# Optimization experiments

Measured on AMD Instinct MI355X. Metric: run time of the kernel, lower is better.

The kernel has to match this reference:

```python
import jax, jax.numpy as jnp
import numpy as np

B, S, TAGSET = 64, 512, 62
T = TAGSET + 2  # + START (index T-2) and END (index T-1)


def setup_inputs() -> dict:
    key = jax.random.key(0)
    k1, k2, k3, k4 = jax.random.split(key, 4)
    feats = jax.random.normal(k1, (B, S, T), dtype=jnp.float32)
    # transitions param (torch init is zeros; small random for a non-degenerate baseline)
    transitions = 0.01 * jax.random.normal(k2, (T, T), dtype=jnp.float32)
    # variable-length contiguous-prefix mask (CRF assumes mask[:, 0] == 1)
    lengths = jax.random.randint(k3, (B,), S // 2, S + 1)
    mask = (jnp.arange(S)[None, :] < lengths[:, None]).astype(jnp.int32)
    tags = jax.random.randint(k4, (B, S), 0, TAGSET).astype(jnp.int32)
    return {"feats": feats, "transitions": transitions, "mask": mask, "tags": tags}


def _nll(feats, transitions, mask, tags):
    b, s, t = feats.shape
    maskb = mask.astype(bool)
    feats_t = jnp.transpose(feats, (1, 0, 2))  # [S, B, T]
    mask_t = jnp.transpose(maskb, (1, 0))       # [S, B]

    # ---- partition function (calculate_PZ) ----
    start = t - 2
    init_part = feats_t[0] + transitions[start][None, :]  # [B, T]

    def step(part, inp):
        f_t, m_t = inp  # f_t: [B, T] emissions, m_t: [B]
        # scores[b, i, j] = part[b, i] + transitions[i, j] + f_t[b, j]
        cur = jax.nn.logsumexp(
            part[:, :, None] + transitions[None, :, :] + f_t[:, None, :], axis=1
        )  # [B, T]
        part = jnp.where(m_t[:, None], cur, part)
        return part, None

    part, _ = jax.lax.scan(step, init_part, (feats_t[1:], mask_t[1:]))
    final = jax.nn.logsumexp(part[:, :, None] + transitions[None, :, :], axis=1)
    forward_score = final[:, t - 1].sum()  # transition into END

    # ---- gold score (score_sentence) ----
    tags = tags.astype(jnp.int32)
    prev = jnp.concatenate(
        [jnp.full((b, 1), start, dtype=jnp.int32), tags[:, :-1]], axis=1
    )  # [B, S] previous tag (START at t=0)
    emit = jnp.take_along_axis(feats, tags[..., None].astype(jnp.int32), axis=2)[..., 0]
    trans = transitions[prev, tags]  # [B, S]
    tg_energy = jnp.where(maskb, emit + trans, 0.0).sum()
    lengths = mask.astype(jnp.int32).sum(axis=1)  # [B]
    end_ids = jnp.take_along_axis(tags, (lengths - 1)[:, None], axis=1)[:, 0]
    end_energy = transitions[end_ids, t - 1].sum()
    gold_score = tg_energy + end_energy

    return forward_score - gold_score


def reference(feats, transitions, mask, tags):
    return _nll(feats, transitions, mask, tags)
```

## Files before the change

### kernel.cpp

```cpp
#include <hip/hip_runtime.h>


#define SS 512
#define TT 64
#define CC 8
#define KCH 64
#define START_TAG 62
#define END_TAG 63
#define LOG2E_F 1.44269504088896340736f
#define LN2_F 0.69314718055994530942f

#define WS_ECOL_OFF 4194304
#define MSTR 72

typedef float v4f __attribute__((ext_vector_type(4)));
typedef _Float16 h4 __attribute__((ext_vector_type(4)));
typedef __fp16 c2 __attribute__((ext_vector_type(2)));
union H4u { h4 v; struct { c2 lo, hi; } p; };

__device__ __forceinline__ void cstep(const h4 (&A)[4][4], h4 (&B)[4],
                                      float* __restrict__ emb, float& fq,
                                      const float* __restrict__ fcol, int tload,
                                      int q, int l, int& esum, int& esc) {
    v4f z = {0.f, 0.f, 0.f, 0.f};
    v4f D[4];
#pragma unroll
    for (int mt = 0; mt < 4; ++mt) {
        v4f a = __builtin_amdgcn_mfma_f32_16x16x16f16(A[mt][0], B[0], z, 0, 0, 0);
        a = __builtin_amdgcn_mfma_f32_16x16x16f16(A[mt][1], B[1], a, 0, 0, 0);
        v4f b = __builtin_amdgcn_mfma_f32_16x16x16f16(A[mt][2], B[2], z, 0, 0, 0);
        b = __builtin_amdgcn_mfma_f32_16x16x16f16(A[mt][3], B[3], b, 0, 0, 0);
        D[mt] = a + b;
    }
    v4f em[4];
#pragma unroll
    for (int mt = 0; mt < 4; ++mt) em[mt] = *(const v4f*)(emb + 16 * mt + 4 * q);
    emb[l] = __builtin_amdgcn_exp2f(fq * LOG2E_F);
    fq = fcol[(size_t)tload * TT];
    esum += esc;
    float scf = __uint_as_float((unsigned)(127 - esc) << 23);
    v4f qs[4];
#pragma unroll
    for (int mt = 0; mt < 4; ++mt) qs[mt] = D[mt] * (em[mt] * scf);
#pragma unroll
    for (int mt = 0; mt < 4; ++mt) {
        H4u u;
        u.p.lo = __builtin_amdgcn_cvt_pkrtz(qs[mt].x, qs[mt].y);
        u.p.hi = __builtin_amdgcn_cvt_pkrtz(qs[mt].z, qs[mt].w);
        B[mt] = u.v;
    }
    unsigned u0 = (unsigned)__builtin_amdgcn_readfirstlane((int)__float_as_uint(qs[0].x));
    esc = (int)((u0 >> 23) & 255u) - 127;
}

__global__ __launch_bounds__(256, 1)
void crf_chunks(const float* __restrict__ feats, const float* __restrict__ trans,
                const int* __restrict__ mask, unsigned short* __restrict__ Pg,
                int* __restrict__ Eg, float* __restrict__ out) {
    __shared__ float em[4][4][2][TT];
    __shared__ __align__(16) _Float16 mldB[TT * MSTR];
    __shared__ __align__(16) _Float16 mldD[TT * MSTR];
    __shared__ int ebuf[12];

    const int blk = blockIdx.x;
    const int chain = blk >> 3, c = blk & 7;
    const int tid = threadIdx.x;
    const int w = tid >> 6, l = tid & 63;
    const int n16 = l & 15, q = l >> 4;
    const int ncol = 16 * w + n16;

    if (blk == 0 && tid == 0) out[0] = 0.f;

    h4 A[4][4];
#pragma unroll
    for (int mt = 0; mt < 4; ++mt)
#pragma unroll
        for (int ks = 0; ks < 4; ++ks) {
            h4 a;
#pragma unroll
            for (int e = 0; e < 4; ++e)
                a[e] = (_Float16)__builtin_amdgcn_exp2f(
                    trans[(16 * ks + 4 * q + e) * TT + 16 * mt + n16] * LOG2E_F);
            A[mt][ks] = a;
        }

    const int* mp = mask + chain * SS;
    int msum = 0;
#pragma unroll
    for (int k = 0; k < 8; ++k) msum += mp[k * 64 + l];
#pragma unroll
    for (int s_ = 1; s_ < 64; s_ <<= 1) msum += __shfl_xor(msum, s_, 64);
    const int L = msum;

    const int t0a = 1 + KCH * c;
    const int t0b = t0a + 16, t0c = t0a + 32, t0d = t0a + 48;
    const int base = (L - 1) - KCH * c;
    int nA = base < 0 ? 0 : (base > 16 ? 16 : base);
    int nB = base - 16 < 0 ? 0 : (base - 16 > 16 ? 16 : base - 16);
    int nC = base - 32 < 0 ? 0 : (base - 32 > 16 ? 16 : base - 32);
    int nD = base - 48 < 0 ? 0 : (base - 48 > 16 ? 16 : base - 48);

    h4 Ba[4], Bb[4], Bc[4], Bd[4];
#pragma unroll
    for (int ks = 0; ks < 4; ++ks) {
        h4 b;
#pragma unroll
        for (int jj = 0; jj < 4; ++jj)
            b[jj] = (_Float16)((16 * ks + 4 * q + jj == ncol) ? 1.f : 0.f);
        Ba[ks] = b; Bb[ks] = b; Bc[ks] = b; Bd[ks] = b;
    }

    const float* fcol = feats + (size_t)chain * SS * TT + l;
#define CT(x) ((x) < SS ? (x) : SS - 1)
    em[0][w][0][l] = __builtin_amdgcn_exp2f(fcol[(size_t)CT(t0a) * TT] * LOG2E_F);
    em[0][w][1][l] = __builtin_amdgcn_exp2f(fcol[(size_t)CT(t0a + 1) * TT] * LOG2E_F);
    em[1][w][0][l] = __builtin_amdgcn_exp2f(fcol[(size_t)CT(t0b) * TT] * LOG2E_F);
    em[1][w][1][l] = __builtin_amdgcn_exp2f(fcol[(size_t)CT(t0b + 1) * TT] * LOG2E_F);
    em[2][w][0][l] = __builtin_amdgcn_exp2f(fcol[(size_t)CT(t0c) * TT] * LOG2E_F);
    em[2][w][1][l] = __builtin_amdgcn_exp2f(fcol[(size_t)CT(t0c + 1) * TT] * LOG2E_F);
    em[3][w][0][l] = __builtin_amdgcn_exp2f(fcol[(size_t)CT(t0d) * TT] * LOG2E_F);
    em[3][w][1][l] = __builtin_amdgcn_exp2f(fcol[(size_t)CT(t0d + 1) * TT] * LOG2E_F);
    float fqA0 = fcol[(size_t)CT(t0a + 2) * TT];
    float fqA1 = fcol[(size_t)CT(t0a + 3) * TT];
    float fqB0 = fcol[(size_t)CT(t0b + 2) * TT];
    float fqB1 = fcol[(size_t)CT(t0b + 3) * TT];
    float fqC0 = fcol[(size_t)CT(t0c + 2) * TT];
    float fqC1 = fcol[(size_t)CT(t0c + 3) * TT];
    float fqD0 = fcol[(size_t)CT(t0d + 2) * TT];
    float fqD1 = fcol[(size_t)CT(t0d + 3) * TT];

    int esA = 0, escA = 0, esB = 0, escB = 0;
    int esC = 0, escC = 0, esD = 0, escD = 0;

    if (nD == 16) {
        for (int r = 0; r < 8; ++r) {
            const int s0 = 2 * r;
            cstep(A, Ba, &em[0][w][0][0], fqA0, fcol, CT(t0a + s0 + 4), q, l, esA, escA);
            cstep(A, Bb, &em[1][w][0][0], fqB0, fcol, CT(t0b + s0 + 4), q, l, esB, escB);
            cstep(A, Bc, &em[2][w][0][0], fqC0, fcol, CT(t0c + s0 + 4), q, l, esC, escC);
            cstep(A, Bd, &em[3][w][0][0], fqD0, fcol, CT(t0d + s0 + 4), q, l, esD, escD);
            cstep(A, Ba, &em[0][w][1][0], fqA1, fcol, CT(t0a + s0 + 5), q, l, esA, escA);
            cstep(A, Bb, &em[1][w][1][0], fqB1, fcol, CT(t0b + s0 + 5), q, l, esB, escB);
            cstep(A, Bc, &em[2][w][1][0], fqC1, fcol, CT(t0c + s0 + 5), q, l, esC, escC);
            cstep(A, Bd, &em[3][w][1][0], fqD1, fcol, CT(t0d + s0 + 5), q, l, esD, escD);
        }
    } else {
        for (int r = 0; r < 8; ++r) {
            const int s0 = 2 * r, s1 = s0 + 1;
            if (s0 < nA) cstep(A, Ba, &em[0][w][0][0], fqA0, fcol, CT(t0a + s0 + 4), q, l, esA, escA);
            if (s0 < nB) cstep(A, Bb, &em[1][w][0][0], fqB0, fcol, CT(t0b + s0 + 4), q, l, esB, escB);
            if (s0 < nC) cstep(A, Bc, &em[2][w][0][0], fqC0, fcol, CT(t0c + s0 + 4), q, l, esC, escC);
            if (s0 < nD) cstep(A, Bd, &em[3][w][0][0], fqD0, fcol, CT(t0d + s0 + 4), q, l, esD, escD);
            if (s1 < nA) cstep(A, Ba, &em[0][w][1][0], fqA1, fcol, CT(t0a + s1 + 4), q, l, esA, escA);
            if (s1 < nB) cstep(A, Bb, &em[1][w][1][0], fqB1, fcol, CT(t0b + s1 + 4), q, l, esB, escB);
            if (s1 < nC) cstep(A, Bc, &em[2][w][1][0], fqC1, fcol, CT(t0c + s1 + 4), q, l, esC, escC);
            if (s1 < nD) cstep(A, Bd, &em[3][w][1][0], fqD1, fcol, CT(t0d + s1 + 4), q, l, esD, escD);
        }
    }
#undef CT

    if (l == 0) { ebuf[w] = esB; ebuf[4 + w] = esD; }
    __syncthreads();
    const int eBmax = max(max(ebuf[0], ebuf[1]), max(ebuf[2], ebuf[3]));
    const int eDmax = max(max(ebuf[4], ebuf[5]), max(ebuf[6], ebuf[7]));
    {
        _Float16 sB = (_Float16)ldexpf(1.f, esB - eBmax);
        _Float16 sD = (_Float16)ldexpf(1.f, esD - eDmax);
        h4 s4B = {sB, sB, sB, sB}, s4D = {sD, sD, sD, sD};
#pragma unroll
        for (int ks = 0; ks < 4; ++ks) {
            h4 vb = Bb[ks] * s4B;
            h4 vd = Bd[ks] * s4D;
#pragma unroll
            for (int jj = 0; jj < 4; ++jj) {
                mldB[(16 * ks + 4 * q + jj) * MSTR + ncol] = vb[jj];
                mldD[(16 * ks + 4 * q + jj) * MSTR + ncol] = vd[jj];
            }
        }
    }
    __syncthreads();
    h4 AHb[4][4], AHd[4][4];
#pragma unroll
    for (int mt = 0; mt < 4; ++mt)
#pragma unroll
        for (int ks = 0; ks < 4; ++ks) {
            AHb[mt][ks] = *(const h4*)(mldB + (16 * mt + n16) * MSTR + 16 * ks + 4 * q);
            AHd[mt][ks] = *(const h4*)(mldD + (16 * mt + n16) * MSTR + 16 * ks + 4 * q);
        }
    v4f z = {0.f, 0.f, 0.f, 0.f};
    v4f P1[4], P2[4];
#pragma unroll
    for (int mt = 0; mt < 4; ++mt) {
        v4f a = __builtin_amdgcn_mfma_f32_16x16x16f16(AHb[mt][0], Ba[0], z, 0, 0, 0);
        a = __builtin_amdgcn_mfma_f32_16x16x16f16(AHb[mt][1], Ba[1], a, 0, 0, 0);
        v4f b = __builtin_amdgcn_mfma_f32_16x16x16f16(AHb[mt][2], Ba[2], z, 0, 0, 0);
        b = __builtin_amdgcn_mfma_f32_16x16x16f16(AHb[mt][3], Ba[3], b, 0, 0, 0);
        P1[mt] = a + b;
        v4f a2 = __builtin_amdgcn_mfma_f32_16x16x16f16(AHd[mt][0], Bc[0], z, 0, 0, 0);
        a2 = __builtin_amdgcn_mfma_f32_16x16x16f16(AHd[mt][1], Bc[1], a2, 0, 0, 0);
        v4f b2 = __builtin_amdgcn_mfma_f32_16x16x16f16(AHd[mt][2], Bc[2], z, 0, 0, 0);
        b2 = __builtin_amdgcn_mfma_f32_16x16x16f16(AHd[mt][3], Bc[3], b2, 0, 0, 0);
        P2[mt] = a2 + b2;
    }
    float m1 = 0.f, m2 = 0.f;
#pragma unroll
    for (int mt = 0; mt < 4; ++mt) {
        m1 = fmaxf(m1, fmaxf(fmaxf(P1[mt].x, P1[mt].y), fmaxf(P1[mt].z, P1[mt].w)));
        m2 = fmaxf(m2, fmaxf(fmaxf(P2[mt].x, P2[mt].y), fmaxf(P2[mt].z, P2[mt].w)));
    }
#pragma unroll
    for (int m = 1; m < 64; m <<= 1) {
        m1 = fmaxf(m1, __shfl_xor(m1, m, 64));
        m2 = fmaxf(m2, __shfl_xor(m2, m, 64));
    }
    unsigned u1 = (unsigned)__builtin_amdgcn_readfirstlane((int)__float_as_uint(m1));
    unsigned u2 = (unsigned)__builtin_amdgcn_readfirstlane((int)__float_as_uint(m2));
    const int e1c = u1 ? (int)((u1 >> 23) & 255u) - 127 : 0;
    const int e2c = u2 ? (int)((u2 >> 23) & 255u) - 127 : 0;
    const int e1 = esA + eBmax + e1c;
    const int e2 = esC + eDmax + e2c;
    h4 P1h[4], P2h[4];
    {
        float s1f = __uint_as_float((unsigned)(127 - e1c) << 23);
        float s2f = __uint_as_float((unsigned)(127 - e2c) << 23);
#pragma unroll
        for (int mt = 0; mt < 4; ++mt) {
            v4f q1 = P1[mt] * s1f;
            v4f q2 = P2[mt] * s2f;
            H4u ua, ub;
            ua.p.lo = __builtin_amdgcn_cvt_pkrtz(q1.x, q1.y);
            ua.p.hi = __builtin_amdgcn_cvt_pkrtz(q1.z, q1.w);
            ub.p.lo = __builtin_amdgcn_cvt_pkrtz(q2.x, q2.y);
            ub.p.hi = __builtin_amdgcn_cvt_pkrtz(q2.z, q2.w);
            P1h[mt] = ua.v;
            P2h[mt] = ub.v;
        }
    }

    if (l == 0) ebuf[8 + w] = e2;
    __syncthreads();
    const int e2max = max(max(ebuf[8], ebuf[9]), max(ebuf[10], ebuf[11]));
    {
        _Float16 s2 = (_Float16)ldexpf(1.f, e2 - e2max);
        h4 s4 = {s2, s2, s2, s2};
#pragma unroll
        for (int mt = 0; mt < 4; ++mt) {
            h4 v = P2h[mt] * s4;
#pragma unroll
            for (int jj = 0; jj < 4; ++jj)
                mldB[(16 * mt + 4 * q + jj) * MSTR + ncol] = v[jj];
        }
    }
    __syncthreads();
    h4 AHp[4][4];
#pragma unroll
    for (int mt = 0; mt < 4; ++mt)
#pragma unroll
        for (int ks = 0; ks < 4; ++ks)
            AHp[mt][ks] = *(const h4*)(mldB + (16 * mt + n16) * MSTR + 16 * ks + 4 * q);
    h4 Rf[4];
#pragma unroll
    for (int mt = 0; mt < 4; ++mt) {
        v4f a = __builtin_amdgcn_mfma_f32_16x16x16f16(AHp[mt][0], P1h[0], z, 0, 0, 0);
        a = __builtin_amdgcn_mfma_f32_16x16x16f16(AHp[mt][1], P1h[1], a, 0, 0, 0);
        v4f b = __builtin_amdgcn_mfma_f32_16x16x16f16(AHp[mt][2], P1h[2], z, 0, 0, 0);
        b = __builtin_amdgcn_mfma_f32_16x16x16f16(AHp[mt][3], P1h[3], b, 0, 0, 0);
        v4f d = a + b;
        H4u u;
        u.p.lo = __builtin_amdgcn_cvt_pkrtz(d.x, d.y);
        u.p.hi = __builtin_amdgcn_cvt_pkrtz(d.z, d.w);
        Rf[mt] = u.v;
    }
#pragma unroll
    for (int mt = 0; mt < 4; ++mt)
#pragma unroll
        for (int jj = 0; jj < 4; ++jj)
            mldD[(16 * mt + 4 * q + jj) * MSTR + ncol] = Rf[mt][jj];
    __syncthreads();
    {
        const size_t base_ = ((size_t)chain * CC + c) * 4096;
        int r = tid >> 2, cb = tid & 3;
        const uint4* src = (const uint4*)(mldD + r * MSTR + cb * 16);
        uint4* dst = (uint4*)(Pg + base_ + r * TT + cb * 16);
        dst[0] = src[0];
        dst[1] = src[1];
    }
    if (q == 0) Eg[(chain * CC + c) * TT + ncol] = e1 + e2max;
}

__global__ __launch_bounds__(64, 1)
void crf_combine(const float* __restrict__ feats, const float* __restrict__ trans,
                 const int* __restrict__ mask, const int* __restrict__ tags,
                 const unsigned short* __restrict__ Pg, const int* __restrict__ Eg,
                 float* __restrict__ out) {
    __shared__ __align__(16) float yl[TT];
    const int chain = blockIdx.x;
    const int j = threadIdx.x;

    int msum = 0;
#pragma unroll
    for (int k = 0; k < 8; ++k) msum += mask[chain * SS + 64 * k + j];
#pragma unroll
    for (int m = 1; m < 64; m <<= 1) msum += __shfl_xor(msum, m, 64);
    const int L = msum;

    float g = 0.f;
#pragma unroll
    for (int k = 0; k < 8; ++k) {
        int t = 64 * k + j;
        if (t < L) {
            int cur = tags[chain * SS + t];
            int prev = t ? tags[chain * SS + t - 1] : START_TAG;
            g += feats[(size_t)chain * SS * TT + (size_t)t * TT + cur] + trans[prev * TT + cur];
        }
    }
#pragma unroll
    for (int m = 1; m < 64; m <<= 1) g += __shfl_xor(g, m, 64);

    float part0 = feats[(size_t)chain * SS * TT + j] + trans[START_TAG * TT + j];
    float M0 = part0;
#pragma unroll
    for (int m = 1; m < 64; m <<= 1) M0 = fmaxf(M0, __shfl_xor(M0, m, 64));
    float x = exp2f((part0 - M0) * LOG2E_F);
    int esumX = 0;

    for (int c = 0; c < CC; ++c) {
        int e = Eg[(chain * CC + c) * TT + j];
        int emax = e;
#pragma unroll
        for (int m = 1; m < 64; m <<= 1) emax = max(emax, __shfl_xor(emax, m, 64));
        yl[j] = ldexpf(x, e - emax);
        float yv[64];
        {
            const uint4* yq = (const uint4*)yl;
#pragma unroll
            for (int i = 0; i < 16; ++i) {
                union { uint4 u; float f[4]; } cv;
                cv.u = yq[i];
                yv[4 * i + 0] = cv.f[0]; yv[4 * i + 1] = cv.f[1];
                yv[4 * i + 2] = cv.f[2]; yv[4 * i + 3] = cv.f[3];
            }
        }
        const uint4* rp = (const uint4*)(Pg + ((size_t)chain * CC + c) * 4096 + (size_t)j * TT);
        float acc = 0.f;
#pragma unroll
        for (int i = 0; i < 8; ++i) {
            union { uint4 u; _Float16 h[8]; } pv;
            pv.u = rp[i];
#pragma unroll
            for (int k2 = 0; k2 < 8; ++k2)
                acc = __builtin_fmaf((float)pv.h[k2], yv[8 * i + k2], acc);
        }
        float am = acc;
#pragma unroll
        for (int m = 1; m < 64; m <<= 1) am = fmaxf(am, __shfl_xor(am, m, 64));
        int e0 = (int)((__float_as_uint(am) >> 23) & 255u) - 127;
        x = ldexpf(acc, -e0);
        esumX += e0 + emax;
    }

    float val = x * expf(trans[j * TT + END_TAG]);
#pragma unroll
    for (int m = 1; m < 64; m <<= 1) val += __shfl_xor(val, m, 64);
    float fwd = logf(val) + (float)esumX * LN2_F + M0;

    if (j == 0) {
        float gold = g + trans[tags[chain * SS + L - 1] * TT + END_TAG];
        atomicAdd(out, fwd - gold);
    }
}

extern "C" void kernel_launch(void* const* d_in, const int* in_sizes, int n_in,
                              void* d_out, int out_size, void* d_ws, size_t ws_size,
                              hipStream_t stream) {
    const float* feats = (const float*)d_in[0];
    const float* trans = (const float*)d_in[1];
    const int*   mask  = (const int*)d_in[2];
    const int*   tags  = (const int*)d_in[3];
    float* out = (float*)d_out;
    unsigned short* Pg = (unsigned short*)d_ws;
    int*       Eg = (int*)((char*)d_ws + WS_ECOL_OFF);

    crf_chunks<<<dim3(64 * CC), dim3(256), 0, stream>>>(feats, trans, mask, Pg, Eg, out);
    crf_combine<<<dim3(64), dim3(64), 0, stream>>>(feats, trans, mask, tags, Pg, Eg, out);
}
```

Before: 113.5 us.

## Combine chunk transfer matrices with an MFMA tree product across four waves

The combine kernel used to apply the eight per-chunk transfer matrices one after another as matrix-vector products in a single 64-thread wave. It now uses 256 threads and pairs chunk matrices with MFMA matrix-matrix products in a tree, staging through LDS and tracking per-column exponent rescaling, before a final reduction against the END weights. This shortens the serial dependency chain and puts the work on the matrix cores. In exchange it does more arithmetic, adds block barriers, and narrows intermediate products to fp16. The diff also leaves a redundant mask reduction and an odd no-op conditional when writing Eg.

Measured after the change: 119.5 us. 1.05x slower.

```diff
diff --git a/kernel.cpp b/kernel.cpp
--- a/kernel.cpp
+++ b/kernel.cpp
@@ -285,87 +285,280 @@
         dst[0] = src[0];
         dst[1] = src[1];
     }
-    if (q == 0) Eg[(chain * CC + c) * TT + ncol] = e1 + e2max;
-}
-
-__global__ __launch_bounds__(64, 1)
+    if (q == 0) Eg[(chain * CC + c) * TT + ncol] = e1 + eBmax == eBmax ? e1 + e2max : e1 + e2max;
+}
+
+__device__ __forceinline__ int wimax64(int v) {
+#pragma unroll
+    for (int m = 1; m < 64; m <<= 1) v = max(v, __shfl_xor(v, m, 64));
+    return v;
+}
+__device__ __forceinline__ float wfmax64(float v) {
+#pragma unroll
+    for (int m = 1; m < 64; m <<= 1) v = fmaxf(v, __shfl_xor(v, m, 64));
+    return v;
+}
+__device__ __forceinline__ float wfsum64(float v) {
+#pragma unroll
+    for (int m = 1; m < 64; m <<= 1) v += __shfl_xor(v, m, 64);
+    return v;
+}
+__device__ __forceinline__ int fexp(float m) {
+    unsigned u = (unsigned)__builtin_amdgcn_readfirstlane((int)__float_as_uint(m));
+    return u ? (int)((u >> 23) & 255u) - 127 : 0;
+}
+__device__ __forceinline__ void mm64(const h4 (&A)[4][4], const h4 (&B)[4], v4f (&D)[4]) {
+    v4f z = {0.f, 0.f, 0.f, 0.f};
+#pragma unroll
+    for (int mt = 0; mt < 4; ++mt) {
+        v4f a = __builtin_amdgcn_mfma_f32_16x16x16f16(A[mt][0], B[0], z, 0, 0, 0);
+        a = __builtin_amdgcn_mfma_f32_16x16x16f16(A[mt][1], B[1], a, 0, 0, 0);
+        v4f b = __builtin_amdgcn_mfma_f32_16x16x16f16(A[mt][2], B[2], z, 0, 0, 0);
+        b = __builtin_amdgcn_mfma_f32_16x16x16f16(A[mt][3], B[3], b, 0, 0, 0);
+        D[mt] = a + b;
+    }
+}
+__device__ __forceinline__ float dmax16(const v4f (&D)[4]) {
+    float m = 0.f;
+#pragma unroll
+    for (int mt = 0; mt < 4; ++mt)
+        m = fmaxf(m, fmaxf(fmaxf(D[mt].x, D[mt].y), fmaxf(D[mt].z, D[mt].w)));
+    return m;
+}
+__device__ __forceinline__ void prodG(const unsigned short* __restrict__ PgC, int cA, int cB,
+                                      const float* __restrict__ sAt,
+                                      int n16, int q, int ncol, v4f (&D)[4]) {
+    const _Float16* Ap = (const _Float16*)PgC + cA * 4096;
+    const _Float16* Bp = (const _Float16*)PgC + cB * 4096;
+    h4 Af[4][4];
+#pragma unroll
+    for (int mt = 0; mt < 4; ++mt)
+#pragma unroll
+        for (int ks = 0; ks < 4; ++ks) {
+            h4 raw = *(const h4*)(Ap + (16 * mt + n16) * TT + 16 * ks + 4 * q);
+            v4f s = *(const v4f*)(sAt + 16 * ks + 4 * q);
+            h4 a;
+#pragma unroll
+            for (int e = 0; e < 4; ++e) a[e] = (_Float16)((float)raw[e] * s[e]);
+            Af[mt][ks] = a;
+        }
+    h4 Bf[4];
+#pragma unroll
+    for (int ks = 0; ks < 4; ++ks) {
+        h4 b;
+#pragma unroll
+        for (int j = 0; j < 4; ++j) b[j] = Bp[(16 * ks + 4 * q + j) * TT + ncol];
+        Bf[ks] = b;
+    }
+    mm64(Af, Bf, D);
+}
+
+__global__ __launch_bounds__(256, 1)
 void crf_combine(const float* __restrict__ feats, const float* __restrict__ trans,
                  const int* __restrict__ mask, const int* __restrict__ tags,
                  const unsigned short* __restrict__ Pg, const int* __restrict__ Eg,
                  float* __restrict__ out) {
-    __shared__ __align__(16) float yl[TT];
+    __shared__ __align__(16) _Float16 stg[TT * MSTR];
+    __shared__ __align__(16) float sA[4][TT];
+    __shared__ __align__(16) float wend[TT];
+    __shared__ int eodd[4];
+    __shared__ int ib0[4], ib1[4], ib2[4], ib3[4];
+    __shared__ float redf[4], gred[4];
+
     const int chain = blockIdx.x;
-    const int j = threadIdx.x;
+    const int tid = threadIdx.x;
+    const int w = tid >> 6, l = tid & 63;
+    const int n16 = l & 15, q = l >> 4;
+    const int ncol = 16 * w + n16;
+    const unsigned short* PgC = Pg + (size_t)chain * CC * 4096;
+    const int* EgC = Eg + chain * CC * TT;
 
     int msum = 0;
 #pragma unroll
-    for (int k = 0; k < 8; ++k) msum += mask[chain * SS + 64 * k + j];
+    for (int k = 0; k < 8; ++k) msum += mask[chain * SS + 64 * k + l];
+    msum = wimax64(msum * 0 + msum);
+    msum = 0;
+#pragma unroll
+    for (int k = 0; k < 8; ++k) msum += mask[chain * SS + 64 * k + l];
 #pragma unroll
     for (int m = 1; m < 64; m <<= 1) msum += __shfl_xor(msum, m, 64);
     const int L = msum;
 
     float g = 0.f;
 #pragma unroll
-    for (int k = 0; k < 8; ++k) {
-        int t = 64 * k + j;
+    for (int rep = 0; rep < 2; ++rep) {
+        int t = tid + rep * 256;
         if (t < L) {
             int cur = tags[chain * SS + t];
             int prev = t ? tags[chain * SS + t - 1] : START_TAG;
             g += feats[(size_t)chain * SS * TT + (size_t)t * TT + cur] + trans[prev * TT + cur];
         }
     }
-#pragma unroll
-    for (int m = 1; m < 64; m <<= 1) g += __shfl_xor(g, m, 64);
-
-    float part0 = feats[(size_t)chain * SS * TT + j] + trans[START_TAG * TT + j];
-    float M0 = part0;
-#pragma unroll
-    for (int m = 1; m < 64; m <<= 1) M0 = fmaxf(M0, __shfl_xor(M0, m, 64));
-    float x = exp2f((part0 - M0) * LOG2E_F);
-    int esumX = 0;
-
-    for (int c = 0; c < CC; ++c) {
-        int e = Eg[(chain * CC + c) * TT + j];
-        int emax = e;
-#pragma unroll
-        for (int m = 1; m < 64; m <<= 1) emax = max(emax, __shfl_xor(emax, m, 64));
-        yl[j] = ldexpf(x, e - emax);
-        float yv[64];
-        {
-            const uint4* yq = (const uint4*)yl;
-#pragma unroll
-            for (int i = 0; i < 16; ++i) {
-                union { uint4 u; float f[4]; } cv;
-                cv.u = yq[i];
-                yv[4 * i + 0] = cv.f[0]; yv[4 * i + 1] = cv.f[1];
-                yv[4 * i + 2] = cv.f[2]; yv[4 * i + 3] = cv.f[3];
-            }
-        }
-        const uint4* rp = (const uint4*)(Pg + ((size_t)chain * CC + c) * 4096 + (size_t)j * TT);
-        float acc = 0.f;
-#pragma unroll
-        for (int i = 0; i < 8; ++i) {
-            union { uint4 u; _Float16 h[8]; } pv;
-            pv.u = rp[i];
-#pragma unroll
-            for (int k2 = 0; k2 < 8; ++k2)
-                acc = __builtin_fmaf((float)pv.h[k2], yv[8 * i + k2], acc);
-        }
-        float am = acc;
-#pragma unroll
-        for (int m = 1; m < 64; m <<= 1) am = fmaxf(am, __shfl_xor(am, m, 64));
-        int e0 = (int)((__float_as_uint(am) >> 23) & 255u) - 127;
-        x = ldexpf(acc, -e0);
-        esumX += e0 + emax;
-    }
-
-    float val = x * expf(trans[j * TT + END_TAG]);
-#pragma unroll
-    for (int m = 1; m < 64; m <<= 1) val += __shfl_xor(val, m, 64);
-    float fwd = logf(val) + (float)esumX * LN2_F + M0;
-
-    if (j == 0) {
-        float gold = g + trans[tags[chain * SS + L - 1] * TT + END_TAG];
+    g = wfsum64(g);
+    if (l == 0) gred[w] = g;
+
+    {
+        int e1 = EgC[(2 * w + 1) * TT + l];
+        int em = wimax64(e1);
+        if (l == 0) eodd[w] = em;
+        sA[w][l] = ldexpf(1.f, e1 - em);
+    }
+    if (tid < TT) wend[tid] = expf(trans[tid * TT + END_TAG]);
+    __syncthreads();
+
+    const float* f0 = feats + (size_t)chain * SS * TT;
+    float pl = f0[l] + trans[START_TAG * TT + l];
+    float M0 = wfmax64(pl);
+    float pc = f0[ncol] + trans[START_TAG * TT + ncol];
+    float p0c = __builtin_amdgcn_exp2f((pc - M0) * LOG2E_F);
+
+    const int eqB0 = EgC[0 * TT + ncol];
+    const int eqB1 = EgC[2 * TT + ncol];
+    const int eqB2 = EgC[4 * TT + ncol];
+    const int eqB3 = EgC[6 * TT + ncol];
+    const int eo0 = eodd[0], eo1 = eodd[1], eo2 = eodd[2], eo3 = eodd[3];
+
+    v4f D[4];
+    prodG(PgC, 3, 2, &sA[1][0], n16, q, ncol, D);
+    int ec1 = fexp(wfmax64(dmax16(D)));
+    int eq1 = eqB1 + eo1 + ec1;
+    if (l == 0) ib0[w] = 0;
+    int eq1m = wimax64(eq1);
+    if (l == 0) ib0[w] = eq1m;
+    __syncthreads();
+    const int emax1 = max(max(ib0[0], ib0[1]), max(ib0[2], ib0[3]));
+    {
+        float sc = ldexpf(1.f, eqB1 + eo1 - emax1);
+#pragma unroll
+        for (int mt = 0; mt < 4; ++mt)
+#pragma unroll
+            for (int jj = 0; jj < 4; ++jj)
+                stg[(16 * mt + 4 * q + jj) * MSTR + ncol] = (_Float16)(D[mt][jj] * sc);
+    }
+    v4f D0[4];
+    prodG(PgC, 1, 0, &sA[0][0], n16, q, ncol, D0);
+    int ec0 = fexp(wfmax64(dmax16(D0)));
+    int eq0 = eqB0 + eo0 + ec0;
+    h4 Q0h[4];
+    {
+        float s0 = ldexpf(1.f, -ec0);
+#pragma unroll
+        for (int mt = 0; mt < 4; ++mt) {
+            v4f qv = D0[mt] * s0;
+            H4u u;
+            u.p.lo = __builtin_amdgcn_cvt_pkrtz(qv.x, qv.y);
+            u.p.hi = __builtin_amdgcn_cvt_pkrtz(qv.z, qv.w);
+            Q0h[mt] = u.v;
+        }
+    }
+    __syncthreads();
+    h4 AH[4][4];
+#pragma unroll
+    for (int mt = 0; mt < 4; ++mt)
+#pragma unroll
+        for (int ks = 0; ks < 4; ++ks)
+            AH[mt][ks] = *(const h4*)(stg + (16 * mt + n16) * MSTR + 16 * ks + 4 * q);
+    v4f Dlo[4];
+    mm64(AH, Q0h, Dlo);
+    int eclo = fexp(wfmax64(dmax16(Dlo)));
+    int eqlo = eq0 + emax1 + eclo;
+    h4 Ploh[4];
+    {
+        float sl = ldexpf(1.f, -eclo);
+#pragma unroll
+        for (int mt = 0; mt < 4; ++mt) {
+            v4f qv = Dlo[mt] * sl;
+            H4u u;
+            u.p.lo = __builtin_amdgcn_cvt_pkrtz(qv.x, qv.y);
+            u.p.hi = __builtin_amdgcn_cvt_pkrtz(qv.z, qv.w);
+            Ploh[mt] = u.v;
+        }
+    }
+    prodG(PgC, 7, 6, &sA[3][0], n16, q, ncol, D);
+    int ec3 = fexp(wfmax64(dmax16(D)));
+    int eq3 = eqB3 + eo3 + ec3;
+    int eq3m = wimax64(eq3);
+    if (l == 0) ib1[w] = eq3m;
+    __syncthreads();
+    const int emax3 = max(max(ib1[0], ib1[1]), max(ib1[2], ib1[3]));
+    {
+        float sc = ldexpf(1.f, eqB3 + eo3 - emax3);
+#pragma unroll
+        for (int mt = 0; mt < 4; ++mt)
+#pragma unroll
+            for (int jj = 0; jj < 4; ++jj)
+                stg[(16 * mt + 4 * q + jj) * MSTR + ncol] = (_Float16)(D[mt][jj] * sc);
+    }
+    v4f D2[4];
+    prodG(PgC, 5, 4, &sA[2][0], n16, q, ncol, D2);
+    int ec2 = fexp(wfmax64(dmax16(D2)));
+    int eq2 = eqB2 + eo2 + ec2;
+    h4 Q2h[4];
+    {
+        float s2 = ldexpf(1.f, -ec2);
+#pragma unroll
+        for (int mt = 0; mt < 4; ++mt) {
+            v4f qv = D2[mt] * s2;
+            H4u u;
+            u.p.lo = __builtin_amdgcn_cvt_pkrtz(qv.x, qv.y);
+            u.p.hi = __builtin_amdgcn_cvt_pkrtz(qv.z, qv.w);
+            Q2h[mt] = u.v;
+        }
+    }
+    __syncthreads();
+#pragma unroll
+    for (int mt = 0; mt < 4; ++mt)
+#pragma unroll
+        for (int ks = 0; ks < 4; ++ks)
+            AH[mt][ks] = *(const h4*)(stg + (16 * mt + n16) * MSTR + 16 * ks + 4 * q);
+    v4f Dhi[4];
+    mm64(AH, Q2h, Dhi);
+    int echi = fexp(wfmax64(dmax16(Dhi)));
+    int eqhi = eq2 + emax3 + echi;
+    int eqhim = wimax64(eqhi);
+    if (l == 0) ib2[w] = eqhim;
+    __syncthreads();
+    const int emaxhi = max(max(ib2[0], ib2[1]), max(ib2[2], ib2[3]));
+    {
+        float sc = ldexpf(1.f, eq2 + emax3 - emaxhi);
+#pragma unroll
+        for (int mt = 0; mt < 4; ++mt)
+#pragma unroll
+            for (int jj = 0; jj < 4; ++jj)
+                stg[(16 * mt + 4 * q + jj) * MSTR + ncol] = (_Float16)(Dhi[mt][jj] * sc);
+    }
+    __syncthreads();
+#pragma unroll
+    for (int mt = 0; mt < 4; ++mt)
+#pragma unroll
+        for (int ks = 0; ks < 4; ++ks)
+            AH[mt][ks] = *(const h4*)(stg + (16 * mt + n16) * MSTR + 16 * ks + 4 * q);
+    v4f DR[4];
+    mm64(AH, Ploh, DR);
+
+    float zsum = 0.f;
+#pragma unroll
+    for (int mt = 0; mt < 4; ++mt) {
+        v4f wv = *(const v4f*)(wend + 16 * mt + 4 * q);
+        zsum += wv.x * DR[mt].x + wv.y * DR[mt].y + wv.z * DR[mt].z + wv.w * DR[mt].w;
+    }
+    zsum += __shfl_xor(zsum, 16, 64);
+    zsum += __shfl_xor(zsum, 32, 64);
+    float val = zsum * p0c;
+    int ex = eqlo + emaxhi;
+    int exm = wimax64(ex);
+    float contrib = (q == 0) ? ldexpf(val, ex - exm) : 0.f;
+    float Sw = wfsum64(contrib);
+    if (l == 0) { redf[w] = Sw; ib3[w] = exm; }
+    __syncthreads();
+    if (tid == 0) {
+        int gmax = max(max(ib3[0], ib3[1]), max(ib3[2], ib3[3]));
+        float tot = 0.f;
+#pragma unroll
+        for (int p = 0; p < 4; ++p) tot += ldexpf(redf[p], ib3[p] - gmax);
+        float fwd = logf(tot) + (float)gmax * LN2_F + M0;
+        float gold = gred[0] + gred[1] + gred[2] + gred[3] +
+                     trans[tags[chain * SS + L - 1] * TT + END_TAG];
         atomicAdd(out, fwd - gold);
     }
 }
@@ -382,5 +575,5 @@
     int*       Eg = (int*)((char*)d_ws + WS_ECOL_OFF);
 
     crf_chunks<<<dim3(64 * CC), dim3(256), 0, stream>>>(feats, trans, mask, Pg, Eg, out);
-    crf_combine<<<dim3(64), dim3(64), 0, stream>>>(feats, trans, mask, tags, Pg, Eg, out);
-}
+    crf_combine<<<dim3(64), dim3(256), 0, stream>>>(feats, trans, mask, tags, Pg, Eg, out);
+}
```

## Halve chunk length to 32, preload emissions to LDS, pipeline combine loads

Applied to the files above, without the earlier changes.

Splits each sequence into 16 chunks of 32 steps instead of 8 of 64, doubling the block count so more chains of matrix steps run in parallel and each block's serial recurrence is shorter. Emission exponentials for the whole chunk are precomputed into shared memory with vectorized loads, replacing per-step global loads inside the recurrence. The combine kernel uses 256 threads for the gold score and double-buffers the per-chunk transfer-matrix rows while doing the chunk products. The cost is twice as many sequential chunk products in combine, twice the workspace, and an extra barrier.

Result: no change. 114.5 us (+0.8%).

```diff
diff --git a/kernel.cpp b/kernel.cpp
--- a/kernel.cpp
+++ b/kernel.cpp
@@ -3,14 +3,14 @@
 
 #define SS 512
 #define TT 64
-#define CC 8
-#define KCH 64
+#define CC 16
+#define KCH 32
 #define START_TAG 62
 #define END_TAG 63
 #define LOG2E_F 1.44269504088896340736f
 #define LN2_F 0.69314718055994530942f
 
-#define WS_ECOL_OFF 4194304
+#define WS_ECOL_OFF 8388608
 #define MSTR 72
 
 typedef float v4f __attribute__((ext_vector_type(4)));
@@ -18,10 +18,9 @@
 typedef __fp16 c2 __attribute__((ext_vector_type(2)));
 union H4u { h4 v; struct { c2 lo, hi; } p; };
 
-__device__ __forceinline__ void cstep(const h4 (&A)[4][4], h4 (&B)[4],
-                                      float* __restrict__ emb, float& fq,
-                                      const float* __restrict__ fcol, int tload,
-                                      int q, int l, int& esum, int& esc) {
+__device__ __forceinline__ void estep(const h4 (&A)[4][4], h4 (&B)[4],
+                                      const float* __restrict__ emrow,
+                                      int q, int& esum, int& esc) {
     v4f z = {0.f, 0.f, 0.f, 0.f};
     v4f D[4];
 #pragma unroll
@@ -32,16 +31,14 @@
         b = __builtin_amdgcn_mfma_f32_16x16x16f16(A[mt][3], B[3], b, 0, 0, 0);
         D[mt] = a + b;
     }
-    v4f em[4];
-#pragma unroll
-    for (int mt = 0; mt < 4; ++mt) em[mt] = *(const v4f*)(emb + 16 * mt + 4 * q);
-    emb[l] = __builtin_amdgcn_exp2f(fq * LOG2E_F);
-    fq = fcol[(size_t)tload * TT];
     esum += esc;
     float scf = __uint_as_float((unsigned)(127 - esc) << 23);
     v4f qs[4];
 #pragma unroll
-    for (int mt = 0; mt < 4; ++mt) qs[mt] = D[mt] * (em[mt] * scf);
+    for (int mt = 0; mt < 4; ++mt) {
+        v4f em = *(const v4f*)(emrow + 16 * mt + 4 * q);
+        qs[mt] = D[mt] * (em * scf);
+    }
 #pragma unroll
     for (int mt = 0; mt < 4; ++mt) {
         H4u u;
@@ -53,17 +50,17 @@
     esc = (int)((u0 >> 23) & 255u) - 127;
 }
 
-__global__ __launch_bounds__(256, 1)
+__global__ __launch_bounds__(256, 4)
 void crf_chunks(const float* __restrict__ feats, const float* __restrict__ trans,
                 const int* __restrict__ mask, unsigned short* __restrict__ Pg,
                 int* __restrict__ Eg, float* __restrict__ out) {
-    __shared__ float em[4][4][2][TT];
+    __shared__ __align__(16) float emS[KCH][TT];
     __shared__ __align__(16) _Float16 mldB[TT * MSTR];
     __shared__ __align__(16) _Float16 mldD[TT * MSTR];
     __shared__ int ebuf[12];
 
     const int blk = blockIdx.x;
-    const int chain = blk >> 3, c = blk & 7;
+    const int chain = blk >> 4, c = blk & 15;
     const int tid = threadIdx.x;
     const int w = tid >> 6, l = tid & 63;
     const int n16 = l & 15, q = l >> 4;
@@ -93,12 +90,28 @@
     const int L = msum;
 
     const int t0a = 1 + KCH * c;
-    const int t0b = t0a + 16, t0c = t0a + 32, t0d = t0a + 48;
     const int base = (L - 1) - KCH * c;
-    int nA = base < 0 ? 0 : (base > 16 ? 16 : base);
-    int nB = base - 16 < 0 ? 0 : (base - 16 > 16 ? 16 : base - 16);
-    int nC = base - 32 < 0 ? 0 : (base - 32 > 16 ? 16 : base - 32);
-    int nD = base - 48 < 0 ? 0 : (base - 48 > 16 ? 16 : base - 48);
+    int nA = base < 0 ? 0 : (base > 8 ? 8 : base);
+    int nB = base - 8 < 0 ? 0 : (base - 8 > 8 ? 8 : base - 8);
+    int nC = base - 16 < 0 ? 0 : (base - 16 > 8 ? 8 : base - 16);
+    int nD = base - 24 < 0 ? 0 : (base - 24 > 8 ? 8 : base - 24);
+
+    const float* fbase = feats + (size_t)chain * SS * TT;
+#pragma unroll
+    for (int k = 0; k < 2; ++k) {
+        int idx = tid + 256 * k;
+        int row = idx >> 4;
+        int seg = idx & 15;
+        int t = t0a + row;
+        t = t < SS ? t : SS - 1;
+        v4f v = *(const v4f*)(fbase + (size_t)t * TT + 4 * seg);
+        v4f e;
+        e.x = __builtin_amdgcn_exp2f(v.x * LOG2E_F);
+        e.y = __builtin_amdgcn_exp2f(v.y * LOG2E_F);
+        e.z = __builtin_amdgcn_exp2f(v.z * LOG2E_F);
+        e.w = __builtin_amdgcn_exp2f(v.w * LOG2E_F);
+        *(v4f*)(&emS[row][4 * seg]) = e;
+    }
 
     h4 Ba[4], Bb[4], Bc[4], Bd[4];
 #pragma unroll
@@ -109,55 +122,36 @@
             b[jj] = (_Float16)((16 * ks + 4 * q + jj == ncol) ? 1.f : 0.f);
         Ba[ks] = b; Bb[ks] = b; Bc[ks] = b; Bd[ks] = b;
     }
-
-    const float* fcol = feats + (size_t)chain * SS * TT + l;
-#define CT(x) ((x) < SS ? (x) : SS - 1)
-    em[0][w][0][l] = __builtin_amdgcn_exp2f(fcol[(size_t)CT(t0a) * TT] * LOG2E_F);
-    em[0][w][1][l] = __builtin_amdgcn_exp2f(fcol[(size_t)CT(t0a + 1) * TT] * LOG2E_F);
-    em[1][w][0][l] = __builtin_amdgcn_exp2f(fcol[(size_t)CT(t0b) * TT] * LOG2E_F);
-    em[1][w][1][l] = __builtin_amdgcn_exp2f(fcol[(size_t)CT(t0b + 1) * TT] * LOG2E_F);
-    em[2][w][0][l] = __builtin_amdgcn_exp2f(fcol[(size_t)CT(t0c) * TT] * LOG2E_F);
-    em[2][w][1][l] = __builtin_amdgcn_exp2f(fcol[(size_t)CT(t0c + 1) * TT] * LOG2E_F);
-    em[3][w][0][l] = __builtin_amdgcn_exp2f(fcol[(size_t)CT(t0d) * TT] * LOG2E_F);
-    em[3][w][1][l] = __builtin_amdgcn_exp2f(fcol[(size_t)CT(t0d + 1) * TT] * LOG2E_F);
-    float fqA0 = fcol[(size_t)CT(t0a + 2) * TT];
-    float fqA1 = fcol[(size_t)CT(t0a + 3) * TT];
-    float fqB0 = fcol[(size_t)CT(t0b + 2) * TT];
-    float fqB1 = fcol[(size_t)CT(t0b + 3) * TT];
-    float fqC0 = fcol[(size_t)CT(t0c + 2) * TT];
-    float fqC1 = fcol[(size_t)CT(t0c + 3) * TT];
-    float fqD0 = fcol[(size_t)CT(t0d + 2) * TT];
-    float fqD1 = fcol[(size_t)CT(t0d + 3) * TT];
+    __syncthreads();
 
     int esA = 0, escA = 0, esB = 0, escB = 0;
     int esC = 0, escC = 0, esD = 0, escD = 0;
 
-    if (nD == 16) {
-        for (int r = 0; r < 8; ++r) {
-            const int s0 = 2 * r;
-            cstep(A, Ba, &em[0][w][0][0], fqA0, fcol, CT(t0a + s0 + 4), q, l, esA, escA);
-            cstep(A, Bb, &em[1][w][0][0], fqB0, fcol, CT(t0b + s0 + 4), q, l, esB, escB);
-            cstep(A, Bc, &em[2][w][0][0], fqC0, fcol, CT(t0c + s0 + 4), q, l, esC, escC);
-            cstep(A, Bd, &em[3][w][0][0], fqD0, fcol, CT(t0d + s0 + 4), q, l, esD, escD);
-            cstep(A, Ba, &em[0][w][1][0], fqA1, fcol, CT(t0a + s0 + 5), q, l, esA, escA);
-            cstep(A, Bb, &em[1][w][1][0], fqB1, fcol, CT(t0b + s0 + 5), q, l, esB, escB);
-            cstep(A, Bc, &em[2][w][1][0], fqC1, fcol, CT(t0c + s0 + 5), q, l, esC, escC);
-            cstep(A, Bd, &em[3][w][1][0], fqD1, fcol, CT(t0d + s0 + 5), q, l, esD, escD);
+    if (nD == 8) {
+        for (int r = 0; r < 4; ++r) {
+            const int s0 = 2 * r, s1 = s0 + 1;
+            estep(A, Ba, &emS[s0][0],      q, esA, escA);
+            estep(A, Bb, &emS[8 + s0][0],  q, esB, escB);
+            estep(A, Bc, &emS[16 + s0][0], q, esC, escC);
+            estep(A, Bd, &emS[24 + s0][0], q, esD, escD);
+            estep(A, Ba, &emS[s1][0],      q, esA, escA);
+            estep(A, Bb, &emS[8 + s1][0],  q, esB, escB);
+            estep(A, Bc, &emS[16 + s1][0], q, esC, escC);
+            estep(A, Bd, &emS[24 + s1][0], q, esD, escD);
         }
     } else {
-        for (int r = 0; r < 8; ++r) {
+        for (int r = 0; r < 4; ++r) {
             const int s0 = 2 * r, s1 = s0 + 1;
-            if (s0 < nA) cstep(A, Ba, &em[0][w][0][0], fqA0, fcol, CT(t0a + s0 + 4), q, l, esA, escA);
-            if (s0 < nB) cstep(A, Bb, &em[1][w][0][0], fqB0, fcol, CT(t0b + s0 + 4), q, l, esB, escB);
-            if (s0 < nC) cstep(A, Bc, &em[2][w][0][0], fqC0, fcol, CT(t0c + s0 + 4), q, l, esC, escC);
-            if (s0 < nD) cstep(A, Bd, &em[3][w][0][0], fqD0, fcol, CT(t0d + s0 + 4), q, l, esD, escD);
-            if (s1 < nA) cstep(A, Ba, &em[0][w][1][0], fqA1, fcol, CT(t0a + s1 + 4), q, l, esA, escA);
-            if (s1 < nB) cstep(A, Bb, &em[1][w][1][0], fqB1, fcol, CT(t0b + s1 + 4), q, l, esB, escB);
-            if (s1 < nC) cstep(A, Bc, &em[2][w][1][0], fqC1, fcol, CT(t0c + s1 + 4), q, l, esC, escC);
-            if (s1 < nD) cstep(A, Bd, &em[3][w][1][0], fqD1, fcol, CT(t0d + s1 + 4), q, l, esD, escD);
-        }
-    }
-#undef CT
+            if (s0 < nA) estep(A, Ba, &emS[s0][0],      q, esA, escA);
+            if (s0 < nB) estep(A, Bb, &emS[8 + s0][0],  q, esB, escB);
+            if (s0 < nC) estep(A, Bc, &emS[16 + s0][0], q, esC, escC);
+            if (s0 < nD) estep(A, Bd, &emS[24 + s0][0], q, esD, escD);
+            if (s1 < nA) estep(A, Ba, &emS[s1][0],      q, esA, escA);
+            if (s1 < nB) estep(A, Bb, &emS[8 + s1][0],  q, esB, escB);
+            if (s1 < nC) estep(A, Bc, &emS[16 + s1][0], q, esC, escC);
+            if (s1 < nD) estep(A, Bd, &emS[24 + s1][0], q, esD, escD);
+        }
+    }
 
     if (l == 0) { ebuf[w] = esB; ebuf[4 + w] = esD; }
     __syncthreads();
@@ -271,6 +265,7 @@
         u.p.hi = __builtin_amdgcn_cvt_pkrtz(d.z, d.w);
         Rf[mt] = u.v;
     }
+    __syncthreads();
 #pragma unroll
     for (int mt = 0; mt < 4; ++mt)
 #pragma unroll
@@ -288,84 +283,122 @@
     if (q == 0) Eg[(chain * CC + c) * TT + ncol] = e1 + e2max;
 }
 
-__global__ __launch_bounds__(64, 1)
+__device__ __forceinline__ int wimax64(int v) {
+#pragma unroll
+    for (int m = 1; m < 64; m <<= 1) v = max(v, __shfl_xor(v, m, 64));
+    return v;
+}
+__device__ __forceinline__ float wfmax64(float v) {
+#pragma unroll
+    for (int m = 1; m < 64; m <<= 1) v = fmaxf(v, __shfl_xor(v, m, 64));
+    return v;
+}
+__device__ __forceinline__ float wfsum64(float v) {
+#pragma unroll
+    for (int m = 1; m < 64; m <<= 1) v += __shfl_xor(v, m, 64);
+    return v;
+}
+__device__ __forceinline__ int fexp(float m) {
+    unsigned u = (unsigned)__builtin_amdgcn_readfirstlane((int)__float_as_uint(m));
+    return u ? (int)((u >> 23) & 255u) - 127 : 0;
+}
+__device__ __forceinline__ void loadrow(uint4 (&h)[8], const unsigned short* __restrict__ PgC,
+                                        int c, int l) {
+    const uint4* rp = (const uint4*)((const _Float16*)PgC + (size_t)c * 4096) + l * 8;
+#pragma unroll
+    for (int i = 0; i < 8; ++i) h[i] = rp[i];
+}
+__device__ __forceinline__ void mvstep(const uint4 (&hv)[8], int e, float* __restrict__ xws,
+                                       int l, float& x, int& exX) {
+    int emax = wimax64(e);
+    float xt = ldexpf(x, e - emax);
+    xws[l] = xt;
+    float acc = 0.f;
+#pragma unroll
+    for (int i = 0; i < 8; ++i) {
+        union { uint4 u; _Float16 hh[8]; } pv;
+        pv.u = hv[i];
+        v4f xa = *(const v4f*)(xws + 8 * i);
+        v4f xb = *(const v4f*)(xws + 8 * i + 4);
+        acc = __builtin_fmaf((float)pv.hh[0], xa.x, acc);
+        acc = __builtin_fmaf((float)pv.hh[1], xa.y, acc);
+        acc = __builtin_fmaf((float)pv.hh[2], xa.z, acc);
+        acc = __builtin_fmaf((float)pv.hh[3], xa.w, acc);
+        acc = __builtin_fmaf((float)pv.hh[4], xb.x, acc);
+        acc = __builtin_fmaf((float)pv.hh[5], xb.y, acc);
+        acc = __builtin_fmaf((float)pv.hh[6], xb.z, acc);
+        acc = __builtin_fmaf((float)pv.hh[7], xb.w, acc);
+    }
+    float am = wfmax64(acc);
+    int e0 = fexp(am);
+    x = ldexpf(acc, -e0);
+    exX += e0 + emax;
+}
+
+__global__ __launch_bounds__(256, 1)
 void crf_combine(const float* __restrict__ feats, const float* __restrict__ trans,
                  const int* __restrict__ mask, const int* __restrict__ tags,
                  const unsigned short* __restrict__ Pg, const int* __restrict__ Eg,
                  float* __restrict__ out) {
-    __shared__ __align__(16) float yl[TT];
+    __shared__ __align__(16) float xsh[4][TT];
+    __shared__ float gred[4];
+
     const int chain = blockIdx.x;
-    const int j = threadIdx.x;
+    const int tid = threadIdx.x;
+    const int w = tid >> 6, l = tid & 63;
+    const unsigned short* PgC = Pg + (size_t)chain * CC * 4096;
+    const int* EgC = Eg + chain * CC * TT;
+    const float* fbase = feats + (size_t)chain * SS * TT;
 
     int msum = 0;
 #pragma unroll
-    for (int k = 0; k < 8; ++k) msum += mask[chain * SS + 64 * k + j];
+    for (int k = 0; k < 8; ++k) msum += mask[chain * SS + 64 * k + l];
 #pragma unroll
     for (int m = 1; m < 64; m <<= 1) msum += __shfl_xor(msum, m, 64);
     const int L = msum;
 
     float g = 0.f;
 #pragma unroll
-    for (int k = 0; k < 8; ++k) {
-        int t = 64 * k + j;
+    for (int rep = 0; rep < 2; ++rep) {
+        int t = tid + rep * 256;
         if (t < L) {
             int cur = tags[chain * SS + t];
             int prev = t ? tags[chain * SS + t - 1] : START_TAG;
-            g += feats[(size_t)chain * SS * TT + (size_t)t * TT + cur] + trans[prev * TT + cur];
-        }
-    }
-#pragma unroll
-    for (int m = 1; m < 64; m <<= 1) g += __shfl_xor(g, m, 64);
-
-    float part0 = feats[(size_t)chain * SS * TT + j] + trans[START_TAG * TT + j];
-    float M0 = part0;
-#pragma unroll
-    for (int m = 1; m < 64; m <<= 1) M0 = fmaxf(M0, __shfl_xor(M0, m, 64));
-    float x = exp2f((part0 - M0) * LOG2E_F);
-    int esumX = 0;
-
-    for (int c = 0; c < CC; ++c) {
-        int e = Eg[(chain * CC + c) * TT + j];
-        int emax = e;
-#pragma unroll
-        for (int m = 1; m < 64; m <<= 1) emax = max(emax, __shfl_xor(emax, m, 64));
-        yl[j] = ldexpf(x, e - emax);
-        float yv[64];
-        {
-            const uint4* yq = (const uint4*)yl;
-#pragma unroll
-            for (int i = 0; i < 16; ++i) {
-                union { uint4 u; float f[4]; } cv;
-                cv.u = yq[i];
-                yv[4 * i + 0] = cv.f[0]; yv[4 * i + 1] = cv.f[1];
-                yv[4 * i + 2] = cv.f[2]; yv[4 * i + 3] = cv.f[3];
-            }
-        }
-        const uint4* rp = (const uint4*)(Pg + ((size_t)chain * CC + c) * 4096 + (size_t)j * TT);
-        float acc = 0.f;
-#pragma unroll
-        for (int i = 0; i < 8; ++i) {
-            union { uint4 u; _Float16 h[8]; } pv;
-            pv.u = rp[i];
-#pragma unroll
-            for (int k2 = 0; k2 < 8; ++k2)
-                acc = __builtin_fmaf((float)pv.h[k2], yv[8 * i + k2], acc);
-        }
-        float am = acc;
-#pragma unroll
-        for (int m = 1; m < 64; m <<= 1) am = fmaxf(am, __shfl_xor(am, m, 64));
-        int e0 = (int)((__float_as_uint(am) >> 23) & 255u) - 127;
-        x = ldexpf(acc, -e0);
-        esumX += e0 + emax;
-    }
-
-    float val = x * expf(trans[j * TT + END_TAG]);
-#pragma unroll
-    for (int m = 1; m < 64; m <<= 1) val += __shfl_xor(val, m, 64);
-    float fwd = logf(val) + (float)esumX * LN2_F + M0;
-
-    if (j == 0) {
-        float gold = g + trans[tags[chain * SS + L - 1] * TT + END_TAG];
+            g += fbase[(size_t)t * TT + cur] + trans[prev * TT + cur];
+        }
+    }
+    g = wfsum64(g);
+    if (l == 0) gred[w] = g;
+
+    float pl = fbase[l] + trans[START_TAG * TT + l];
+    float M0 = wfmax64(pl);
+    float x = __builtin_amdgcn_exp2f((pl - M0) * LOG2E_F);
+    int exX = 0;
+
+    uint4 hA[8], hB[8];
+    int eA, eB;
+    loadrow(hA, PgC, 0, l);
+    eA = EgC[0 * TT + l];
+#pragma unroll
+    for (int c = 0; c < CC; c += 2) {
+        loadrow(hB, PgC, c + 1, l);
+        eB = EgC[(c + 1) * TT + l];
+        mvstep(hA, eA, &xsh[w][0], l, x, exX);
+        if (c + 2 < CC) {
+            loadrow(hA, PgC, c + 2, l);
+            eA = EgC[(c + 2) * TT + l];
+        }
+        mvstep(hB, eB, &xsh[w][0], l, x, exX);
+    }
+
+    float val = x * expf(trans[l * TT + END_TAG]);
+    val = wfsum64(val);
+    float fwd = logf(val) + (float)exX * LN2_F + M0;
+
+    __syncthreads();
+    if (tid == 0) {
+        float gold = gred[0] + gred[1] + gred[2] + gred[3] +
+                     trans[tags[chain * SS + L - 1] * TT + END_TAG];
         atomicAdd(out, fwd - gold);
     }
 }
@@ -382,5 +415,5 @@
     int*       Eg = (int*)((char*)d_ws + WS_ECOL_OFF);
 
     crf_chunks<<<dim3(64 * CC), dim3(256), 0, stream>>>(feats, trans, mask, Pg, Eg, out);
-    crf_combine<<<dim3(64), dim3(64), 0, stream>>>(feats, trans, mask, tags, Pg, Eg, out);
-}
+    crf_combine<<<dim3(64), dim3(256), 0, stream>>>(feats, trans, mask, tags, Pg, Eg, out);
+}
```
